# Optimization experiments

Hardware: AMD Instinct MI355X
Metric: run time of the kernel (lower is better)

Reference implementation:

```python
import jax, jax.numpy as jnp
import numpy as np

PAD, UNK, START = 0, 1, 2
V, E, H = 32000, 256, 512   # vocab, emb dim, encoder hidden per direction
H2 = 2 * H                   # decoder hidden / encoder output dim
B, L, T = 32, 400, 64
OOV = 100


def _lstm(xe, Wi, Wh, b, reverse=False):
    """xe: [B,L,E] -> (hs [B,L,H], h_last [B,H])."""
    Bb = xe.shape[0]
    Hh = Wh.shape[0]
    def step(carry, xt):
        h, c = carry
        z = xt @ Wi + h @ Wh + b
        i, fg, g, o = jnp.split(z, 4, axis=-1)
        c = jax.nn.sigmoid(fg) * c + jax.nn.sigmoid(i) * jnp.tanh(g)
        h = jax.nn.sigmoid(o) * jnp.tanh(c)
        return (h, c), h
    init = (jnp.zeros((Bb, Hh), xe.dtype), jnp.zeros((Bb, Hh), xe.dtype))
    (hN, _), hs = jax.lax.scan(step, init, jnp.swapaxes(xe, 0, 1), reverse=reverse)
    return jnp.swapaxes(hs, 0, 1), hN


def _gru(x, h, Wi, Wh, b):
    D = h.shape[-1]
    zi = x @ Wi + b
    zh = h @ Wh
    r = jax.nn.sigmoid(zi[:, :D] + zh[:, :D])
    z = jax.nn.sigmoid(zi[:, D:2 * D] + zh[:, D:2 * D])
    n = jnp.tanh(zi[:, 2 * D:] + r * zh[:, 2 * D:])
    return (1.0 - z) * n + z * h


def _forward(embedding, enc_Wi_f, enc_Wh_f, enc_b_f, enc_Wi_b, enc_Wh_b, enc_b_b,
             dec_Wi, dec_Wh, dec_b, W_enc_att, W_dec_att, Wv, bv, Wp, bp,
             x, target_y, extend_vocab):
    Bb, Ll = x.shape
    Tt = target_y.shape[1]
    Vv = embedding.shape[0]
    Hh2 = dec_Wh.shape[0]
    xe = embedding[x]                                           # B,L,E
    hs_f, hN_f = _lstm(xe, enc_Wi_f, enc_Wh_f, enc_b_f)
    hs_b, hN_b = _lstm(xe, enc_Wi_b, enc_Wh_b, enc_b_b, reverse=True)
    enc_out = jnp.concatenate([hs_f, hs_b], axis=-1)            # B,L,2H
    dec_h0 = jnp.concatenate([hN_f, hN_b], axis=-1)             # B,2H
    bidx = jnp.arange(Bb)[:, None]

    def step(carry, inp):
        dec_in, dec_h, acc, prebuf = carry
        i, tgt = inp
        emb = embedding[dec_in]                                 # B,E
        dec_h = _gru(emb, dec_h, dec_Wi, dec_Wh, dec_b)         # B,2H
        # temporal encoder attention (normalize exp scores by running sum)
        e = jnp.einsum('bh,hk,blk->bl', dec_h, W_enc_att, enc_out)
        ee = jnp.exp(e)
        att_un = jnp.where(i == 0, ee, ee / (acc + 1e-10))
        acc = acc + ee
        enc_att = att_un / jnp.sum(att_un, axis=-1, keepdims=True)   # B,L
        enc_ctx = jnp.einsum('bl,blh->bh', enc_att, enc_out)
        # intra-decoder attention over previous decoder hiddens
        ed = jnp.einsum('bh,hk,btk->bt', dec_h, W_dec_att, prebuf)
        dmask = (jnp.arange(prebuf.shape[1]) < i)[None, :]
        dec_att = jax.nn.softmax(jnp.where(dmask, ed, -1e9), axis=-1)
        dec_ctx = jnp.einsum('bt,bth->bh', dec_att, prebuf)
        dec_ctx = jnp.where(i > 0, dec_ctx, 0.0)
        cat = jnp.concatenate([dec_h, enc_ctx, dec_ctx], axis=-1)    # B,6H
        p_gen = jax.nn.sigmoid(cat @ Wp + bp)                        # B,1
        ptr_dist = p_gen * enc_att                                   # B,L
        vocab_dist = (1.0 - p_gen) * jax.nn.softmax(cat @ Wv + bv, axis=-1)
        final = jnp.zeros((Bb, Vv + OOV), vocab_dist.dtype)
        final = final.at[:, :Vv].set(vocab_dist)
        final = final.at[bidx, extend_vocab].add(ptr_dist)           # copy mechanism
        dec_out = jnp.argmax(final, axis=-1)
        step_loss = -jnp.log(final[jnp.arange(Bb), tgt] + 1e-12)
        step_loss = step_loss * (tgt != PAD).astype(final.dtype)
        prebuf = jax.lax.dynamic_update_slice(prebuf, dec_h[:, None, :], (0, i, 0))
        nxt = jnp.where(dec_out >= Vv, UNK, dec_out).astype(dec_in.dtype)
        return (nxt, dec_h, acc, prebuf), (dec_out, step_loss)

    init = (jnp.full((Bb,), START, dtype=x.dtype), dec_h0,
            jnp.zeros((Bb, Ll), enc_out.dtype),
            jnp.zeros((Bb, Tt, Hh2), enc_out.dtype))
    _, (ys, losses) = jax.lax.scan(step, init, (jnp.arange(Tt), target_y.T))
    return jnp.swapaxes(ys, 0, 1), jnp.swapaxes(losses, 0, 1)


def setup_inputs() -> dict:
    key = jax.random.key(0)
    ks = jax.random.split(key, 16)
    s = 0.02
    nrm = lambda k, shape: jax.random.normal(k, shape, jnp.float32) * s
    return {
        'x': jax.random.randint(ks[0], (B, L), 0, V),
        'seq_len': L,
        'target_y': jax.random.randint(ks[1], (B, T), 0, V),
        'extend_vocab': jax.random.randint(ks[2], (B, L), 0, V + OOV),
        'max_ovv_len': OOV,
        'embedding': nrm(ks[3], (V, E)),
        'enc_Wi_f': nrm(ks[4], (E, 4 * H)),
        'enc_Wh_f': nrm(ks[5], (H, 4 * H)),
        'enc_b_f': jnp.zeros((4 * H,), jnp.float32),
        'enc_Wi_b': nrm(ks[6], (E, 4 * H)),
        'enc_Wh_b': nrm(ks[7], (H, 4 * H)),
        'enc_b_b': jnp.zeros((4 * H,), jnp.float32),
        'dec_Wi': nrm(ks[8], (E, 3 * H2)),
        'dec_Wh': nrm(ks[9], (H2, 3 * H2)),
        'dec_b': jnp.zeros((3 * H2,), jnp.float32),
        'W_enc_att': nrm(ks[10], (H2, H2)),
        'W_dec_att': nrm(ks[11], (H2, H2)),
        'Wv': nrm(ks[12], (3 * H2, V)),
        'bv': jnp.zeros((V,), jnp.float32),
        'Wp': nrm(ks[13], (3 * H2, 1)),
        'bp': jnp.zeros((1,), jnp.float32),
    }


def reference(x, seq_len, target_y, extend_vocab, max_ovv_len,
              embedding, enc_Wi_f, enc_Wh_f, enc_b_f, enc_Wi_b, enc_Wh_b, enc_b_b,
              dec_Wi, dec_Wh, dec_b, W_enc_att, W_dec_att, Wv, bv, Wp, bp):
    return _forward(embedding, enc_Wi_f, enc_Wh_f, enc_b_f, enc_Wi_b, enc_Wh_b, enc_b_b,
                    dec_Wi, dec_Wh, dec_b, W_enc_att, W_dec_att, Wv, bv, Wp, bp,
                    x, target_y, extend_vocab)
```

## Files before the change

kernel.cpp:

```cpp
#include <hip/hip_runtime.h>
#include <math.h>

#define Bb 32
#define Lmax 400
#define Tt 64
#define Ee 256
#define Hh 512
#define H2 1024
#define Vv 32000
#define OOV 100
#define VX (Vv+OOV)
#define PAD_ID 0
#define UNK_ID 1
#define START_ID 2

__device__ __forceinline__ float sigf(float x){ return 1.0f/(1.0f+expf(-x)); }
__device__ __forceinline__ float bf2f(unsigned int u){ u <<= 16; return __uint_as_float(u); }

__global__ __launch_bounds__(256) void pack_enc_k(
    const float* __restrict__ Wi_f, const float* __restrict__ Wh_f, const float* __restrict__ b_f,
    const float* __restrict__ Wi_b, const float* __restrict__ Wh_b, const float* __restrict__ b_b,
    float4* __restrict__ wip, float4* __restrict__ whp, float4* __restrict__ bp)
{
  int o = blockIdx.x*256 + threadIdx.x;
  if (o < 2*256*512) {
    int n = o & 511; int k = (o >> 9) & 255; int dir = o >> 17;
    const float* W = dir ? Wi_b : Wi_f;
    wip[o] = make_float4(W[k*2048+n], W[k*2048+512+n], W[k*2048+1024+n], W[k*2048+1536+n]);
  }
  if (o < 2*512*512) {
    int n = o & 511; int k = (o >> 9) & 511; int dir = o >> 18;
    const float* W = dir ? Wh_b : Wh_f;
    whp[o] = make_float4(W[k*2048+n], W[k*2048+512+n], W[k*2048+1024+n], W[k*2048+1536+n]);
  }
  if (o < 2*512) {
    int n = o & 511; int dir = o >> 9;
    const float* bs = dir ? b_b : b_f;
    bp[o] = make_float4(bs[n], bs[512+n], bs[1024+n], bs[1536+n]);
  }
}

__global__ __launch_bounds__(512) void enc_step2_k(
    const float4* __restrict__ wip, const float4* __restrict__ whp, const float4* __restrict__ bp,
    const float* __restrict__ emb, const int* __restrict__ x,
    float* __restrict__ c_buf, float* __restrict__ enc_out, int t)
{
  __shared__ float4 wi_s[256*4];
  __shared__ float4 wh_s[512*4];
  __shared__ float4 red_s[4*128];
  int bx = blockIdx.x;
  int dir = bx >> 7, ng = bx & 127;
  int tid = threadIdx.x;
  int b = tid & 31, nl = (tid >> 5) & 3, ks = tid >> 7;
  int n = ng*4 + nl;
  for (int i = tid; i < 1024; i += 512) {
    int k = i >> 2, l = i & 3;
    wi_s[i] = wip[(dir*256 + k)*512 + ng*4 + l];
  }
  for (int i = tid; i < 2048; i += 512) {
    int k = i >> 2, l = i & 3;
    wh_s[i] = whp[(dir*512 + k)*512 + ng*4 + l];
  }
  __syncthreads();
  int tt = dir ? (Lmax-1-t) : t;
  int tok = x[b*Lmax + tt];
  const float* xr = emb + (size_t)tok*Ee;
  float4 acc = make_float4(0.f,0.f,0.f,0.f);
  if (t > 0) {
    int pt = dir ? (tt+1) : (tt-1);
    const float4* hb4 = (const float4*)(enc_out + ((size_t)b*Lmax + pt)*H2 + dir*Hh);
    #pragma unroll 4
    for (int k4 = ks*32; k4 < ks*32+32; ++k4) {
      float4 hv = hb4[k4];
      float4 w0 = wh_s[(k4*4+0)*4 + nl];
      float4 w1 = wh_s[(k4*4+1)*4 + nl];
      float4 w2 = wh_s[(k4*4+2)*4 + nl];
      float4 w3 = wh_s[(k4*4+3)*4 + nl];
      acc.x = fmaf(hv.x,w0.x,acc.x); acc.y = fmaf(hv.x,w0.y,acc.y);
      acc.z = fmaf(hv.x,w0.z,acc.z); acc.w = fmaf(hv.x,w0.w,acc.w);
      acc.x = fmaf(hv.y,w1.x,acc.x); acc.y = fmaf(hv.y,w1.y,acc.y);
      acc.z = fmaf(hv.y,w1.z,acc.z); acc.w = fmaf(hv.y,w1.w,acc.w);
      acc.x = fmaf(hv.z,w2.x,acc.x); acc.y = fmaf(hv.z,w2.y,acc.y);
      acc.z = fmaf(hv.z,w2.z,acc.z); acc.w = fmaf(hv.z,w2.w,acc.w);
      acc.x = fmaf(hv.w,w3.x,acc.x); acc.y = fmaf(hv.w,w3.y,acc.y);
      acc.z = fmaf(hv.w,w3.z,acc.z); acc.w = fmaf(hv.w,w3.w,acc.w);
    }
  }
  const float4* xr4 = (const float4*)xr;
  #pragma unroll 4
  for (int k4 = ks*16; k4 < ks*16+16; ++k4) {
    float4 xv = xr4[k4];
    float4 w0 = wi_s[(k4*4+0)*4 + nl];
    float4 w1 = wi_s[(k4*4+1)*4 + nl];
    float4 w2 = wi_s[(k4*4+2)*4 + nl];
    float4 w3 = wi_s[(k4*4+3)*4 + nl];
    acc.x = fmaf(xv.x,w0.x,acc.x); acc.y = fmaf(xv.x,w0.y,acc.y);
    acc.z = fmaf(xv.x,w0.z,acc.z); acc.w = fmaf(xv.x,w0.w,acc.w);
    acc.x = fmaf(xv.y,w1.x,acc.x); acc.y = fmaf(xv.y,w1.y,acc.y);
    acc.z = fmaf(xv.y,w1.z,acc.z); acc.w = fmaf(xv.y,w1.w,acc.w);
    acc.x = fmaf(xv.z,w2.x,acc.x); acc.y = fmaf(xv.z,w2.y,acc.y);
    acc.z = fmaf(xv.z,w2.z,acc.z); acc.w = fmaf(xv.z,w2.w,acc.w);
    acc.x = fmaf(xv.w,w3.x,acc.x); acc.y = fmaf(xv.w,w3.y,acc.y);
    acc.z = fmaf(xv.w,w3.z,acc.z); acc.w = fmaf(xv.w,w3.w,acc.w);
  }
  red_s[ks*128 + (tid & 127)] = acc;
  __syncthreads();
  if (tid < 128) {
    float4 a0 = red_s[tid], a1 = red_s[128+tid], a2 = red_s[256+tid], a3 = red_s[384+tid];
    float4 bb = bp[dir*512 + n];
    float zi = a0.x+a1.x+a2.x+a3.x + bb.x;
    float zf = a0.y+a1.y+a2.y+a3.y + bb.y;
    float zg = a0.z+a1.z+a2.z+a3.z + bb.z;
    float zo = a0.w+a1.w+a2.w+a3.w + bb.w;
    int ci = (dir*32 + b)*Hh + n;
    float cv = (t==0) ? 0.f : c_buf[ci];
    float cn = sigf(zf)*cv + sigf(zi)*tanhf(zg);
    float hn = sigf(zo)*tanhf(cn);
    c_buf[ci] = cn;
    enc_out[((size_t)b*Lmax + tt)*H2 + dir*Hh + n] = hn;
  }
}

__global__ __launch_bounds__(256) void init_dec_k(
    const float* __restrict__ enc_out, float* __restrict__ cat_buf, int* __restrict__ dec_in)
{
  int idx = blockIdx.x*256 + threadIdx.x;
  if (idx < Bb*H2) {
    int b = idx >> 10, n = idx & 1023;
    float v = (n < Hh) ? enc_out[((size_t)b*Lmax + (Lmax-1))*H2 + n]
                       : enc_out[(size_t)b*Lmax*H2 + n];
    cat_buf[b*3*H2 + n] = v;
  }
  if (idx < Bb) dec_in[idx] = START_ID;
}

__global__ __launch_bounds__(256) void gru_mm_k(
    const float* __restrict__ emb, const int* __restrict__ dec_in,
    const float* __restrict__ cat_buf, const float* __restrict__ Wi,
    const float* __restrict__ Wh, const float* __restrict__ bias,
    float* __restrict__ zi_buf, float* __restrict__ zh_buf)
{
  int bx = blockIdx.x;
  int ng = bx % 48; int bg = (bx / 48) & 7; int kq = bx / 384;
  int nl = threadIdx.x & 63, bl = threadIdx.x >> 6;
  int n = ng*64 + nl, b = bg*4 + bl;
  const float* hr = cat_buf + b*3*H2;
  float zh = 0.f;
  int k0 = kq*512;
  #pragma unroll 4
  for (int k = k0; k < k0+512; ++k)
    zh = fmaf(hr[k], Wh[(size_t)k*3*H2 + n], zh);
  zh_buf[(size_t)(kq*Bb + b)*3*H2 + n] = zh;
  if (kq == 0) {
    const float* er = emb + (size_t)dec_in[b]*Ee;
    float zi = bias[n];
    #pragma unroll 4
    for (int k = 0; k < Ee; ++k)
      zi = fmaf(er[k], Wi[(size_t)k*3*H2 + n], zi);
    zi_buf[b*3*H2 + n] = zi;
  }
}

__global__ __launch_bounds__(256) void gru_comb_k(
    const float* __restrict__ zi_buf, const float* __restrict__ zh_buf,
    float* __restrict__ cat_buf, float* __restrict__ prebuf, int t)
{
  int idx = blockIdx.x*256 + threadIdx.x;
  int b = idx >> 10, n = idx & 1023;
  const float* zi  = zi_buf + b*3*H2;
  const float* zh0 = zh_buf + (size_t)b*3*H2;
  const float* zh1 = zh_buf + (size_t)(Bb + b)*3*H2;
  float zhr = zh0[n]      + zh1[n];
  float zhz = zh0[H2+n]   + zh1[H2+n];
  float zhg = zh0[2*H2+n] + zh1[2*H2+n];
  float r  = sigf(zi[n] + zhr);
  float z  = sigf(zi[H2+n] + zhz);
  float nn = tanhf(zi[2*H2+n] + r*zhg);
  float hold = cat_buf[b*3*H2 + n];
  float h = (1.0f - z)*nn + z*hold;
  cat_buf[b*3*H2 + n] = h;
  prebuf[((size_t)b*Tt + t)*H2 + n] = h;
}

__global__ __launch_bounds__(256) void qq_k(
    const float* __restrict__ cat_buf, const float* __restrict__ Wea,
    const float* __restrict__ Wda, float* __restrict__ qp, float* __restrict__ qdp)
{
  int bx = blockIdx.x;
  int ng = bx & 15, bg = (bx >> 4) & 7, kq = bx >> 7;
  int nl = threadIdx.x & 63, bl = threadIdx.x >> 6;
  int n = ng*64 + nl, b = bg*4 + bl;
  const float* hr = cat_buf + b*3*H2 + kq*256;
  const float* wa = Wea + (size_t)(kq*256)*H2 + n;
  const float* wd = Wda + (size_t)(kq*256)*H2 + n;
  float s1 = 0.f, s2 = 0.f;
  #pragma unroll 4
  for (int k = 0; k < 256; ++k) {
    float hv = hr[k];
    s1 = fmaf(hv, wa[(size_t)k*H2], s1);
    s2 = fmaf(hv, wd[(size_t)k*H2], s2);
  }
  qp [(size_t)(kq*Bb + b)*H2 + n] = s1;
  qdp[(size_t)(kq*Bb + b)*H2 + n] = s2;
}

__global__ __launch_bounds__(256) void att_sc_k(
    const float* __restrict__ qp, const float* __restrict__ qdp,
    const float* __restrict__ enc_out, const float* __restrict__ prebuf,
    float* __restrict__ esc, float* __restrict__ ed, int t)
{
  int w = blockIdx.x*4 + (threadIdx.x >> 6);
  int lane = threadIdx.x & 63;
  int b = w / 464;
  int row = w - b*464;
  if (b >= Bb) return;
  float s = 0.0f;
  if (row < Lmax) {
    const float4* q0 = (const float4*)(qp + (size_t)(0*Bb + b)*H2);
    const float4* q1 = (const float4*)(qp + (size_t)(1*Bb + b)*H2);
    const float4* q2 = (const float4*)(qp + (size_t)(2*Bb + b)*H2);
    const float4* q3 = (const float4*)(qp + (size_t)(3*Bb + b)*H2);
    const float4* er = (const float4*)(enc_out + ((size_t)b*Lmax + row)*H2);
    #pragma unroll
    for (int j = 0; j < 4; ++j) {
      int idx = lane + 64*j;
      float4 a0 = q0[idx], a1 = q1[idx], a2 = q2[idx], a3 = q3[idx], e = er[idx];
      float ax = a0.x+a1.x+a2.x+a3.x;
      float ay = a0.y+a1.y+a2.y+a3.y;
      float az = a0.z+a1.z+a2.z+a3.z;
      float aw = a0.w+a1.w+a2.w+a3.w;
      s += ax*e.x + ay*e.y + az*e.z + aw*e.w;
    }
  } else {
    int tp = row - Lmax;
    if (tp >= t) { if (lane==0) ed[b*Tt+tp] = 0.0f; return; }
    const float4* q0 = (const float4*)(qdp + (size_t)(0*Bb + b)*H2);
    const float4* q1 = (const float4*)(qdp + (size_t)(1*Bb + b)*H2);
    const float4* q2 = (const float4*)(qdp + (size_t)(2*Bb + b)*H2);
    const float4* q3 = (const float4*)(qdp + (size_t)(3*Bb + b)*H2);
    const float4* pr = (const float4*)(prebuf + ((size_t)b*Tt + tp)*H2);
    #pragma unroll
    for (int j = 0; j < 4; ++j) {
      int idx = lane + 64*j;
      float4 a0 = q0[idx], a1 = q1[idx], a2 = q2[idx], a3 = q3[idx], e = pr[idx];
      float ax = a0.x+a1.x+a2.x+a3.x;
      float ay = a0.y+a1.y+a2.y+a3.y;
      float az = a0.z+a1.z+a2.z+a3.z;
      float aw = a0.w+a1.w+a2.w+a3.w;
      s += ax*e.x + ay*e.y + az*e.z + aw*e.w;
    }
  }
  for (int o = 32; o > 0; o >>= 1) s += __shfl_xor(s, o);
  if (lane == 0) { if (row < Lmax) esc[b*Lmax+row] = s; else ed[b*Tt + (row-Lmax)] = s; }
}

__global__ __launch_bounds__(256) void ctx_norm_k(
    const float* __restrict__ esc, const float* __restrict__ acc_r, float* __restrict__ acc_w,
    float* __restrict__ enc_att, const float* __restrict__ ed,
    const float* __restrict__ enc_out, const float* __restrict__ prebuf,
    float* __restrict__ cat_buf, int t)
{
  __shared__ float att_s[Lmax];
  __shared__ float datt_s[Tt];
  __shared__ float red[256];
  int b = blockIdx.x >> 4, kq = blockIdx.x & 15;
  int tid = threadIdx.x;
  float loc = 0.f;
  for (int l = tid; l < Lmax; l += 256) {
    float ee = expf(esc[b*Lmax + l]);
    float a  = (t == 0) ? 0.f : acc_r[b*Lmax + l];
    float un = (t == 0) ? ee : ee / (a + 1e-10f);
    att_s[l] = un;
    loc += un;
    if (kq == 0) acc_w[b*Lmax + l] = a + ee;
  }
  red[tid] = loc; __syncthreads();
  for (int s = 128; s > 0; s >>= 1) { if (tid < s) red[tid] += red[tid+s]; __syncthreads(); }
  float inv = 1.0f / red[0];
  for (int l = tid; l < Lmax; l += 256) {
    float v = att_s[l] * inv;
    att_s[l] = v;
    if (kq == 0) enc_att[b*Lmax + l] = v;
  }
  if (tid < 64 && t > 0) {
    float v = (tid < t) ? ed[b*Tt + tid] : -INFINITY;
    float m = v;
    for (int o = 32; o > 0; o >>= 1) m = fmaxf(m, __shfl_xor(m, o));
    float p = (tid < t) ? expf(v - m) : 0.f;
    float ss = p;
    for (int o = 32; o > 0; o >>= 1) ss += __shfl_xor(ss, o);
    datt_s[tid] = p / ss;
  }
  __syncthreads();
  int k = kq*64 + (tid & 63);
  int strip = tid >> 6;
  float ec = 0.f;
  const float* er = enc_out + (size_t)b*Lmax*H2 + k;
  #pragma unroll 4
  for (int l = strip; l < Lmax; l += 4)
    ec = fmaf(att_s[l], er[(size_t)l*H2], ec);
  float dc = 0.f;
  const float* pr = prebuf + (size_t)b*Tt*H2 + k;
  for (int tp = strip; tp < t; tp += 4)
    dc = fmaf(datt_s[tp], pr[(size_t)tp*H2], dc);
  __syncthreads();
  red[tid] = ec; __syncthreads();
  if (tid < 64)
    cat_buf[b*3*H2 + H2 + kq*64 + tid] = red[tid] + red[64+tid] + red[128+tid] + red[192+tid];
  __syncthreads();
  red[tid] = dc; __syncthreads();
  if (tid < 64)
    cat_buf[b*3*H2 + 2*H2 + kq*64 + tid] = red[tid] + red[64+tid] + red[128+tid] + red[192+tid];
}

__global__ __launch_bounds__(256) void pack_wv_k(const float* __restrict__ Wv, unsigned short* __restrict__ Wbf)
{
  size_t i = ((size_t)blockIdx.x*256 + threadIdx.x)*4;
  #pragma unroll
  for (int j = 0; j < 4; ++j) {
    unsigned int u = __float_as_uint(Wv[i+j]);
    u = (u + 0x7fffu + ((u >> 16) & 1u)) >> 16;
    Wbf[i+j] = (unsigned short)u;
  }
}

__global__ __launch_bounds__(256) void wv_mm_bf_k(
    const float* __restrict__ cat_buf, const unsigned short* __restrict__ Wbf,
    const float* __restrict__ bv, float* __restrict__ logits)
{
  __shared__ float As[32][33];
  __shared__ float Wsh[32][65];
  int tid = threadIdx.x;
  int n0 = blockIdx.x*64;
  int tx = tid & 15, ty = tid >> 4;
  float acc[2][4] = {};
  for (int k0 = 0; k0 < 3*H2; k0 += 32) {
    #pragma unroll
    for (int i = 0; i < 4; ++i) {
      int a = tid*4+i;
      As[a>>5][a&31] = cat_buf[(size_t)(a>>5)*3*H2 + k0 + (a&31)];
    }
    #pragma unroll
    for (int j = 0; j < 4; ++j) {
      int a = j*256 + tid;
      int row = a >> 5, c2 = (a & 31)*2;
      const unsigned int* wr = (const unsigned int*)(Wbf + (size_t)(k0+row)*Vv + n0);
      unsigned int u = wr[a & 31];
      Wsh[row][c2]   = bf2f(u & 0xffffu);
      Wsh[row][c2+1] = bf2f(u >> 16);
    }
    __syncthreads();
    #pragma unroll
    for (int kk = 0; kk < 32; ++kk) {
      float a0 = As[ty*2+0][kk], a1 = As[ty*2+1][kk];
      float w0 = Wsh[kk][tx*4+0], w1 = Wsh[kk][tx*4+1], w2 = Wsh[kk][tx*4+2], w3 = Wsh[kk][tx*4+3];
      acc[0][0]=fmaf(a0,w0,acc[0][0]); acc[0][1]=fmaf(a0,w1,acc[0][1]); acc[0][2]=fmaf(a0,w2,acc[0][2]); acc[0][3]=fmaf(a0,w3,acc[0][3]);
      acc[1][0]=fmaf(a1,w0,acc[1][0]); acc[1][1]=fmaf(a1,w1,acc[1][1]); acc[1][2]=fmaf(a1,w2,acc[1][2]); acc[1][3]=fmaf(a1,w3,acc[1][3]);
    }
    __syncthreads();
  }
  #pragma unroll
  for (int i = 0; i < 2; ++i)
    #pragma unroll
    for (int j = 0; j < 4; ++j) {
      int n = n0 + tx*4 + j;
      logits[(size_t)(ty*2+i)*Vv + n] = acc[i][j] + bv[n];
    }
}

__global__ __launch_bounds__(256) void wv_mm_k(
    const float* __restrict__ cat_buf, const float* __restrict__ Wv,
    const float* __restrict__ bv, float* __restrict__ logits)
{
  __shared__ float As[32][33];
  __shared__ float Wsh[32][128];
  int tid = threadIdx.x;
  int n0 = blockIdx.x*128;
  int tx = tid & 31, ty = tid >> 5;
  float acc[4][4] = {};
  for (int k0 = 0; k0 < 3*H2; k0 += 32) {
    #pragma unroll
    for (int i = 0; i < 4; ++i) {
      int a = tid*4+i;
      As[a>>5][a&31] = cat_buf[(size_t)(a>>5)*3*H2 + k0 + (a&31)];
    }
    #pragma unroll
    for (int j = 0; j < 16; ++j) {
      int a = j*256+tid;
      Wsh[a>>7][a&127] = Wv[(size_t)(k0+(a>>7))*Vv + n0 + (a&127)];
    }
    __syncthreads();
    #pragma unroll
    for (int kk = 0; kk < 32; ++kk) {
      float a0 = As[ty*4+0][kk], a1 = As[ty*4+1][kk], a2 = As[ty*4+2][kk], a3 = As[ty*4+3][kk];
      float w0 = Wsh[kk][tx*4+0], w1 = Wsh[kk][tx*4+1], w2 = Wsh[kk][tx*4+2], w3 = Wsh[kk][tx*4+3];
      acc[0][0]=fmaf(a0,w0,acc[0][0]); acc[0][1]=fmaf(a0,w1,acc[0][1]); acc[0][2]=fmaf(a0,w2,acc[0][2]); acc[0][3]=fmaf(a0,w3,acc[0][3]);
      acc[1][0]=fmaf(a1,w0,acc[1][0]); acc[1][1]=fmaf(a1,w1,acc[1][1]); acc[1][2]=fmaf(a1,w2,acc[1][2]); acc[1][3]=fmaf(a1,w3,acc[1][3]);
      acc[2][0]=fmaf(a2,w0,acc[2][0]); acc[2][1]=fmaf(a2,w1,acc[2][1]); acc[2][2]=fmaf(a2,w2,acc[2][2]); acc[2][3]=fmaf(a2,w3,acc[2][3]);
      acc[3][0]=fmaf(a3,w0,acc[3][0]); acc[3][1]=fmaf(a3,w1,acc[3][1]); acc[3][2]=fmaf(a3,w2,acc[3][2]); acc[3][3]=fmaf(a3,w3,acc[3][3]);
    }
    __syncthreads();
  }
  #pragma unroll
  for (int i = 0; i < 4; ++i)
    #pragma unroll
    for (int j = 0; j < 4; ++j) {
      int n = n0 + tx*4 + j;
      logits[(size_t)(ty*4+i)*Vv + n] = acc[i][j] + bv[n];
    }
}

__global__ __launch_bounds__(256) void final_k(
    const float* __restrict__ logits, const float* __restrict__ cat_buf,
    const float* __restrict__ Wp, const float* __restrict__ bps,
    const int* __restrict__ ev, const float* __restrict__ enc_att,
    const int* __restrict__ tgt_y, float* __restrict__ out,
    int* __restrict__ dec_in, int t)
{
  __shared__ float rf[256];
  __shared__ int   ri[256];
  __shared__ float tm[256];
  __shared__ int   ev_s[Lmax];
  __shared__ float pv_s[Lmax];
  __shared__ float m_sh, sc_sh, pg_sh;
  int b = blockIdx.x, tid = threadIdx.x;
  const float*  lr  = logits + (size_t)b*Vv;
  const float4* lr4 = (const float4*)lr;
  {
    const float* catr = cat_buf + b*3*H2;
    float pgl = 0.f;
    for (int i = tid; i < 3*H2; i += 256) pgl += catr[i]*Wp[i];
    rf[tid] = pgl; __syncthreads();
    for (int s = 128; s > 0; s >>= 1) { if (tid < s) rf[tid] += rf[tid+s]; __syncthreads(); }
    if (tid == 0) pg_sh = sigf(rf[0] + bps[0]);
    __syncthreads();
  }
  float m = -1e30f;
  for (int i = tid; i < Vv/4; i += 256) {
    float4 v = lr4[i];
    m = fmaxf(m, fmaxf(fmaxf(v.x,v.y), fmaxf(v.z,v.w)));
  }
  rf[tid] = m; __syncthreads();
  for (int s = 128; s > 0; s >>= 1) { if (tid < s) rf[tid] = fmaxf(rf[tid], rf[tid+s]); __syncthreads(); }
  m = rf[0]; __syncthreads();
  float ssum = 0.f;
  for (int i = tid; i < Vv/4; i += 256) {
    float4 v = lr4[i];
    ssum += expf(v.x-m) + expf(v.y-m) + expf(v.z-m) + expf(v.w-m);
  }
  rf[tid] = ssum; __syncthreads();
  for (int s = 128; s > 0; s >>= 1) { if (tid < s) rf[tid] += rf[tid+s]; __syncthreads(); }
  if (tid == 0) {
    sc_sh = (1.0f - pg_sh) / rf[0]; m_sh = m;
  }
  for (int l = tid; l < Lmax; l += 256) ev_s[l] = ev[b*Lmax + l];
  __syncthreads();
  float scale = sc_sh, pg = pg_sh; m = m_sh;
  for (int l = tid; l < Lmax; l += 256) pv_s[l] = pg * enc_att[b*Lmax + l];
  __syncthreads();
  float best = -1e30f; int bi = 0x7fffffff;
  for (int i = tid; i < Vv/4; i += 256) {
    float4 v = lr4[i];
    float p0 = expf(v.x-m)*scale, p1 = expf(v.y-m)*scale, p2 = expf(v.z-m)*scale, p3 = expf(v.w-m)*scale;
    int n = 4*i;
    if (p0 > best) { best = p0; bi = n; }
    if (p1 > best || (p1 == best && n+1 < bi)) { best = p1; bi = n+1; }
    if (p2 > best || (p2 == best && n+2 < bi)) { best = p2; bi = n+2; }
    if (p3 > best || (p3 == best && n+3 < bi)) { best = p3; bi = n+3; }
  }
  int tgt = tgt_y[b*Tt + t];
  float ptm = 0.f;
  for (int l = tid; l < Lmax; l += 256) {
    int e = ev_s[l];
    float tot = 0.f;
    for (int l2 = 0; l2 < Lmax; ++l2) if (ev_s[l2] == e) tot += pv_s[l2];
    float vvv = tot + ((e < Vv) ? expf(lr[e]-m)*scale : 0.f);
    if (vvv > best || (vvv == best && e < bi)) { best = vvv; bi = e; }
    ptm += (e == tgt) ? pv_s[l] : 0.f;
  }
  rf[tid] = best; ri[tid] = bi; tm[tid] = ptm; __syncthreads();
  for (int s = 128; s > 0; s >>= 1) {
    if (tid < s) {
      float v2 = rf[tid+s]; int i2 = ri[tid+s];
      if (v2 > rf[tid] || (v2 == rf[tid] && i2 < ri[tid])) { rf[tid] = v2; ri[tid] = i2; }
      tm[tid] += tm[tid+s];
    }
    __syncthreads();
  }
  if (tid == 0) {
    int am = ri[0];
    float fr_tgt = expf(lr[tgt]-m)*scale + tm[0];
    float loss = (tgt != PAD_ID) ? -logf(fr_tgt + 1e-12f) : 0.0f;
    out[b*Tt + t] = (float)am;
    out[Bb*Tt + b*Tt + t] = loss;
    dec_in[b] = (am >= Vv) ? UNK_ID : am;
  }
}

extern "C" void kernel_launch(void* const* d_in, const int* in_sizes, int n_in,
                              void* d_out, int out_size, void* d_ws, size_t ws_size,
                              hipStream_t stream)
{
  const int*   x    = (const int*)  d_in[0];
  const int*   tgt  = (const int*)  d_in[2];
  const int*   ev   = (const int*)  d_in[3];
  const float* emb  = (const float*)d_in[5];
  const float* Wi_f = (const float*)d_in[6];
  const float* Wh_f = (const float*)d_in[7];
  const float* b_f  = (const float*)d_in[8];
  const float* Wi_b = (const float*)d_in[9];
  const float* Wh_b = (const float*)d_in[10];
  const float* b_b  = (const float*)d_in[11];
  const float* dWi  = (const float*)d_in[12];
  const float* dWh  = (const float*)d_in[13];
  const float* db   = (const float*)d_in[14];
  const float* Wea  = (const float*)d_in[15];
  const float* Wda  = (const float*)d_in[16];
  const float* Wv   = (const float*)d_in[17];
  const float* bv   = (const float*)d_in[18];
  const float* Wp   = (const float*)d_in[19];
  const float* bp   = (const float*)d_in[20];
  float* out = (float*)d_out;

  float* ws = (float*)d_ws;
  size_t off = 0;
  float* enc_out = ws + off; off += (size_t)Bb*Lmax*H2;
  float* c_buf   = ws + off; off += 2*Bb*Hh;
  float4* wip    = (float4*)(ws + off); off += 2*256*512*4;
  float4* whp    = (float4*)(ws + off); off += 2*512*512*4;
  float4* biasp  = (float4*)(ws + off); off += 2*512*4;
  float* cat_buf = ws + off; off += Bb*3*H2;
  float* prebuf  = ws + off; off += (size_t)Bb*Tt*H2;
  float* accumA  = ws + off; off += Bb*Lmax;
  float* accumB  = ws + off; off += Bb*Lmax;
  float* zi_buf  = ws + off; off += Bb*3*H2;
  float* zh_buf  = ws + off; off += (size_t)2*Bb*3*H2;
  float* qp      = ws + off; off += (size_t)4*Bb*H2;
  float* qdp     = ws + off; off += (size_t)4*Bb*H2;
  float* esc     = ws + off; off += Bb*Lmax;
  float* enc_att = ws + off; off += Bb*Lmax;
  float* ed      = ws + off; off += Bb*Tt;
  float* logits  = ws + off; off += (size_t)Bb*Vv;
  int*   dec_in  = (int*)(ws + off); off += 32;
  unsigned short* Wbf = (unsigned short*)(ws + off);
  size_t need_bf16 = off*4 + (size_t)3*H2*Vv*2;
  int use_bf16 = (ws_size >= need_bf16 + (64u<<10)) ? 1 : 0;

  pack_enc_k<<<2048,256,0,stream>>>(Wi_f,Wh_f,b_f,Wi_b,Wh_b,b_b,wip,whp,biasp);
  if (use_bf16) pack_wv_k<<<96000,256,0,stream>>>(Wv, Wbf);

  for (int t = 0; t < Lmax; ++t)
    enc_step2_k<<<256,512,0,stream>>>(wip,whp,biasp,emb,x,c_buf,enc_out,t);

  init_dec_k<<<128,256,0,stream>>>(enc_out,cat_buf,dec_in);

  for (int t = 0; t < Tt; ++t) {
    float* ar = (t & 1) ? accumB : accumA;
    float* aw = (t & 1) ? accumA : accumB;
    gru_mm_k  <<<768,256,0,stream>>>(emb,dec_in,cat_buf,dWi,dWh,db,zi_buf,zh_buf);
    gru_comb_k<<<128,256,0,stream>>>(zi_buf,zh_buf,cat_buf,prebuf,t);
    qq_k      <<<512,256,0,stream>>>(cat_buf,Wea,Wda,qp,qdp);
    att_sc_k  <<<3712,256,0,stream>>>(qp,qdp,enc_out,prebuf,esc,ed,t);
    ctx_norm_k<<<512,256,0,stream>>>(esc,ar,aw,enc_att,ed,enc_out,prebuf,cat_buf,t);
    if (use_bf16) wv_mm_bf_k<<<500,256,0,stream>>>(cat_buf,Wbf,bv,logits);
    else          wv_mm_k   <<<250,256,0,stream>>>(cat_buf,Wv,bv,logits);
    final_k   <<<32,256,0,stream>>>(logits,cat_buf,Wp,bp,ev,enc_att,tgt,out,dec_in,t);
  }
}
```

Before: 37.15 ms.

## Register-tile encoder LSTM step over batch and fuse GRU combine into attention projection

The encoder step kernel now stages the previous hidden states and embeddings for all 32 batch rows in shared memory. Each thread computes 4 batch rows and reuses each loaded weight float4 across them, with a 16-way k-split reduction through shared memory. The GRU combine kernel is folded into the query-projection kernel, which recomputes the new hidden state per block, and a small qsum kernel pre-reduces the four k-split partial projections. This removes redundant partial sums in the 3712-block attention-score kernel. The costs are more shared memory per encoder block, which may limit occupancy, and redundant GRU gate computation across the 16 column groups.

```diff
diff --git a/kernel.cpp b/kernel.cpp
--- a/kernel.cpp
+++ b/kernel.cpp
@@ -40,19 +40,34 @@
   }
 }
 
-__global__ __launch_bounds__(512) void enc_step2_k(
+#define FMA16(ACC, HV, W0, W1, W2, W3) \
+  ACC.x = fmaf(HV.x, W0.x, ACC.x); ACC.y = fmaf(HV.x, W0.y, ACC.y); \
+  ACC.z = fmaf(HV.x, W0.z, ACC.z); ACC.w = fmaf(HV.x, W0.w, ACC.w); \
+  ACC.x = fmaf(HV.y, W1.x, ACC.x); ACC.y = fmaf(HV.y, W1.y, ACC.y); \
+  ACC.z = fmaf(HV.y, W1.z, ACC.z); ACC.w = fmaf(HV.y, W1.w, ACC.w); \
+  ACC.x = fmaf(HV.z, W2.x, ACC.x); ACC.y = fmaf(HV.z, W2.y, ACC.y); \
+  ACC.z = fmaf(HV.z, W2.z, ACC.z); ACC.w = fmaf(HV.z, W2.w, ACC.w); \
+  ACC.x = fmaf(HV.w, W3.x, ACC.x); ACC.y = fmaf(HV.w, W3.y, ACC.y); \
+  ACC.z = fmaf(HV.w, W3.z, ACC.z); ACC.w = fmaf(HV.w, W3.w, ACC.w);
+
+__global__ __launch_bounds__(512) void enc_step3_k(
     const float4* __restrict__ wip, const float4* __restrict__ whp, const float4* __restrict__ bp,
     const float* __restrict__ emb, const int* __restrict__ x,
     float* __restrict__ c_buf, float* __restrict__ enc_out, int t)
 {
   __shared__ float4 wi_s[256*4];
   __shared__ float4 wh_s[512*4];
-  __shared__ float4 red_s[4*128];
+  __shared__ float4 hs2[128*33];
+  __shared__ float4 xr_red[64*33];
   int bx = blockIdx.x;
   int dir = bx >> 7, ng = bx & 127;
   int tid = threadIdx.x;
-  int b = tid & 31, nl = (tid >> 5) & 3, ks = tid >> 7;
-  int n = ng*4 + nl;
+  int ks = tid >> 5;
+  int r  = tid & 31;
+  int bq = r & 7, nl = r >> 3;
+  int b0 = bq*4;
+  int tt = dir ? (Lmax-1-t) : t;
+
   for (int i = tid; i < 1024; i += 512) {
     int k = i >> 2, l = i & 3;
     wi_s[i] = wip[(dir*256 + k)*512 + ng*4 + l];
@@ -61,57 +76,91 @@
     int k = i >> 2, l = i & 3;
     wh_s[i] = whp[(dir*512 + k)*512 + ng*4 + l];
   }
-  __syncthreads();
-  int tt = dir ? (Lmax-1-t) : t;
-  int tok = x[b*Lmax + tt];
-  const float* xr = emb + (size_t)tok*Ee;
-  float4 acc = make_float4(0.f,0.f,0.f,0.f);
+  {
+    int sb = tid >> 4, kb = tid & 15;
+    int tok = x[sb*Lmax + tt];
+    const float4* er = (const float4*)(emb + (size_t)tok*Ee);
+    #pragma unroll
+    for (int i = 0; i < 4; ++i) {
+      int k4 = kb + 16*i;
+      xr_red[k4*33 + sb] = er[k4];
+    }
+  }
   if (t > 0) {
     int pt = dir ? (tt+1) : (tt-1);
-    const float4* hb4 = (const float4*)(enc_out + ((size_t)b*Lmax + pt)*H2 + dir*Hh);
-    #pragma unroll 4
-    for (int k4 = ks*32; k4 < ks*32+32; ++k4) {
-      float4 hv = hb4[k4];
+    int sb = tid >> 4, kb = tid & 15;
+    const float4* hb = (const float4*)(enc_out + ((size_t)sb*Lmax + pt)*H2 + dir*Hh);
+    #pragma unroll
+    for (int i = 0; i < 8; ++i) {
+      int k4 = kb + 16*i;
+      hs2[k4*33 + sb] = hb[k4];
+    }
+  }
+  __syncthreads();
+
+  float4 acc0 = make_float4(0.f,0.f,0.f,0.f);
+  float4 acc1 = acc0, acc2 = acc0, acc3 = acc0;
+  if (t > 0) {
+    int k4b = ks*8;
+    #pragma unroll
+    for (int kk = 0; kk < 8; ++kk) {
+      int k4 = k4b + kk;
       float4 w0 = wh_s[(k4*4+0)*4 + nl];
       float4 w1 = wh_s[(k4*4+1)*4 + nl];
       float4 w2 = wh_s[(k4*4+2)*4 + nl];
       float4 w3 = wh_s[(k4*4+3)*4 + nl];
-      acc.x = fmaf(hv.x,w0.x,acc.x); acc.y = fmaf(hv.x,w0.y,acc.y);
-      acc.z = fmaf(hv.x,w0.z,acc.z); acc.w = fmaf(hv.x,w0.w,acc.w);
-      acc.x = fmaf(hv.y,w1.x,acc.x); acc.y = fmaf(hv.y,w1.y,acc.y);
-      acc.z = fmaf(hv.y,w1.z,acc.z); acc.w = fmaf(hv.y,w1.w,acc.w);
-      acc.x = fmaf(hv.z,w2.x,acc.x); acc.y = fmaf(hv.z,w2.y,acc.y);
-      acc.z = fmaf(hv.z,w2.z,acc.z); acc.w = fmaf(hv.z,w2.w,acc.w);
-      acc.x = fmaf(hv.w,w3.x,acc.x); acc.y = fmaf(hv.w,w3.y,acc.y);
-      acc.z = fmaf(hv.w,w3.z,acc.z); acc.w = fmaf(hv.w,w3.w,acc.w);
-    }
-  }
-  const float4* xr4 = (const float4*)xr;
-  #pragma unroll 4
-  for (int k4 = ks*16; k4 < ks*16+16; ++k4) {
-    float4 xv = xr4[k4];
-    float4 w0 = wi_s[(k4*4+0)*4 + nl];
-    float4 w1 = wi_s[(k4*4+1)*4 + nl];
-    float4 w2 = wi_s[(k4*4+2)*4 + nl];
-    float4 w3 = wi_s[(k4*4+3)*4 + nl];
-    acc.x = fmaf(xv.x,w0.x,acc.x); acc.y = fmaf(xv.x,w0.y,acc.y);
-    acc.z = fmaf(xv.x,w0.z,acc.z); acc.w = fmaf(xv.x,w0.w,acc.w);
-    acc.x = fmaf(xv.y,w1.x,acc.x); acc.y = fmaf(xv.y,w1.y,acc.y);
-    acc.z = fmaf(xv.y,w1.z,acc.z); acc.w = fmaf(xv.y,w1.w,acc.w);
-    acc.x = fmaf(xv.z,w2.x,acc.x); acc.y = fmaf(xv.z,w2.y,acc.y);
-    acc.z = fmaf(xv.z,w2.z,acc.z); acc.w = fmaf(xv.z,w2.w,acc.w);
-    acc.x = fmaf(xv.w,w3.x,acc.x); acc.y = fmaf(xv.w,w3.y,acc.y);
-    acc.z = fmaf(xv.w,w3.z,acc.z); acc.w = fmaf(xv.w,w3.w,acc.w);
-  }
-  red_s[ks*128 + (tid & 127)] = acc;
+      float4 h0 = hs2[k4*33 + b0+0];
+      float4 h1 = hs2[k4*33 + b0+1];
+      float4 h2 = hs2[k4*33 + b0+2];
+      float4 h3 = hs2[k4*33 + b0+3];
+      FMA16(acc0, h0, w0, w1, w2, w3);
+      FMA16(acc1, h1, w0, w1, w2, w3);
+      FMA16(acc2, h2, w0, w1, w2, w3);
+      FMA16(acc3, h3, w0, w1, w2, w3);
+    }
+  }
+  {
+    int k4b = ks*4;
+    #pragma unroll
+    for (int kk = 0; kk < 4; ++kk) {
+      int k4 = k4b + kk;
+      float4 w0 = wi_s[(k4*4+0)*4 + nl];
+      float4 w1 = wi_s[(k4*4+1)*4 + nl];
+      float4 w2 = wi_s[(k4*4+2)*4 + nl];
+      float4 w3 = wi_s[(k4*4+3)*4 + nl];
+      float4 h0 = xr_red[k4*33 + b0+0];
+      float4 h1 = xr_red[k4*33 + b0+1];
+      float4 h2 = xr_red[k4*33 + b0+2];
+      float4 h3 = xr_red[k4*33 + b0+3];
+      FMA16(acc0, h0, w0, w1, w2, w3);
+      FMA16(acc1, h1, w0, w1, w2, w3);
+      FMA16(acc2, h2, w0, w1, w2, w3);
+      FMA16(acc3, h3, w0, w1, w2, w3);
+    }
+  }
+  __syncthreads();
+  {
+    int base = ks*132 + 16*bq + nl;
+    xr_red[base + 0]  = acc0;
+    xr_red[base + 4]  = acc1;
+    xr_red[base + 8]  = acc2;
+    xr_red[base + 12] = acc3;
+  }
   __syncthreads();
   if (tid < 128) {
-    float4 a0 = red_s[tid], a1 = red_s[128+tid], a2 = red_s[256+tid], a3 = red_s[384+tid];
+    int bn = tid;
+    float4 s = xr_red[bn];
+    #pragma unroll
+    for (int kr = 1; kr < 16; ++kr) {
+      float4 v = xr_red[kr*132 + bn];
+      s.x += v.x; s.y += v.y; s.z += v.z; s.w += v.w;
+    }
+    int b = bn >> 2, nl2 = bn & 3, n = ng*4 + nl2;
     float4 bb = bp[dir*512 + n];
-    float zi = a0.x+a1.x+a2.x+a3.x + bb.x;
-    float zf = a0.y+a1.y+a2.y+a3.y + bb.y;
-    float zg = a0.z+a1.z+a2.z+a3.z + bb.z;
-    float zo = a0.w+a1.w+a2.w+a3.w + bb.w;
+    float zi = s.x + bb.x;
+    float zf = s.y + bb.y;
+    float zg = s.z + bb.z;
+    float zo = s.w + bb.w;
     int ci = (dir*32 + b)*Hh + n;
     float cv = (t==0) ? 0.f : c_buf[ci];
     float cn = sigf(zf)*cv + sigf(zi)*tanhf(zg);
@@ -122,7 +171,8 @@
 }
 
 __global__ __launch_bounds__(256) void init_dec_k(
-    const float* __restrict__ enc_out, float* __restrict__ cat_buf, int* __restrict__ dec_in)
+    const float* __restrict__ enc_out, float* __restrict__ cat_buf,
+    float* __restrict__ h0, int* __restrict__ dec_in)
 {
   int idx = blockIdx.x*256 + threadIdx.x;
   if (idx < Bb*H2) {
@@ -130,6 +180,7 @@
     float v = (n < Hh) ? enc_out[((size_t)b*Lmax + (Lmax-1))*H2 + n]
                        : enc_out[(size_t)b*Lmax*H2 + n];
     cat_buf[b*3*H2 + n] = v;
+    h0[b*H2 + n] = v;
   }
   if (idx < Bb) dec_in[idx] = START_ID;
 }
@@ -161,51 +212,70 @@
   }
 }
 
-__global__ __launch_bounds__(256) void gru_comb_k(
+__global__ __launch_bounds__(256) void qq_f_k(
     const float* __restrict__ zi_buf, const float* __restrict__ zh_buf,
-    float* __restrict__ cat_buf, float* __restrict__ prebuf, int t)
-{
-  int idx = blockIdx.x*256 + threadIdx.x;
-  int b = idx >> 10, n = idx & 1023;
-  const float* zi  = zi_buf + b*3*H2;
-  const float* zh0 = zh_buf + (size_t)b*3*H2;
-  const float* zh1 = zh_buf + (size_t)(Bb + b)*3*H2;
-  float zhr = zh0[n]      + zh1[n];
-  float zhz = zh0[H2+n]   + zh1[H2+n];
-  float zhg = zh0[2*H2+n] + zh1[2*H2+n];
-  float r  = sigf(zi[n] + zhr);
-  float z  = sigf(zi[H2+n] + zhz);
-  float nn = tanhf(zi[2*H2+n] + r*zhg);
-  float hold = cat_buf[b*3*H2 + n];
-  float h = (1.0f - z)*nn + z*hold;
-  cat_buf[b*3*H2 + n] = h;
-  prebuf[((size_t)b*Tt + t)*H2 + n] = h;
-}
-
-__global__ __launch_bounds__(256) void qq_k(
-    const float* __restrict__ cat_buf, const float* __restrict__ Wea,
-    const float* __restrict__ Wda, float* __restrict__ qp, float* __restrict__ qdp)
-{
+    const float* __restrict__ h0, float* __restrict__ prebuf,
+    const float* __restrict__ Wea, const float* __restrict__ Wda,
+    float* __restrict__ cat_buf, float* __restrict__ qp, float* __restrict__ qdp, int t)
+{
+  __shared__ float hsq[4*260];
   int bx = blockIdx.x;
   int ng = bx & 15, bg = (bx >> 4) & 7, kq = bx >> 7;
   int nl = threadIdx.x & 63, bl = threadIdx.x >> 6;
   int n = ng*64 + nl, b = bg*4 + bl;
-  const float* hr = cat_buf + b*3*H2 + kq*256;
+  const float* zi  = zi_buf + b*3*H2;
+  const float* zh0 = zh_buf + (size_t)b*3*H2;
+  const float* zh1 = zh_buf + (size_t)(Bb + b)*3*H2;
+  #pragma unroll
+  for (int i = 0; i < 4; ++i) {
+    int kk = nl + 64*i, k = kq*256 + kk;
+    float zhr = zh0[k]      + zh1[k];
+    float zhz = zh0[H2+k]   + zh1[H2+k];
+    float zhg = zh0[2*H2+k] + zh1[2*H2+k];
+    float rr = sigf(zi[k] + zhr);
+    float zz = sigf(zi[H2+k] + zhz);
+    float nn = tanhf(zi[2*H2+k] + rr*zhg);
+    float hold = (t == 0) ? h0[b*H2 + k]
+                          : prebuf[((size_t)b*Tt + (t-1))*H2 + k];
+    float h = (1.0f - zz)*nn + zz*hold;
+    hsq[bl*260 + kk] = h;
+    if (ng == 0) {
+      cat_buf[b*3*H2 + k] = h;
+      prebuf[((size_t)b*Tt + t)*H2 + k] = h;
+    }
+  }
+  __syncthreads();
+  const float* hr = hsq + bl*260;
   const float* wa = Wea + (size_t)(kq*256)*H2 + n;
   const float* wd = Wda + (size_t)(kq*256)*H2 + n;
   float s1 = 0.f, s2 = 0.f;
   #pragma unroll 4
-  for (int k = 0; k < 256; ++k) {
-    float hv = hr[k];
-    s1 = fmaf(hv, wa[(size_t)k*H2], s1);
-    s2 = fmaf(hv, wd[(size_t)k*H2], s2);
+  for (int kk = 0; kk < 256; ++kk) {
+    float hv = hr[kk];
+    s1 = fmaf(hv, wa[(size_t)kk*H2], s1);
+    s2 = fmaf(hv, wd[(size_t)kk*H2], s2);
   }
   qp [(size_t)(kq*Bb + b)*H2 + n] = s1;
   qdp[(size_t)(kq*Bb + b)*H2 + n] = s2;
 }
 
+__global__ __launch_bounds__(256) void qsum_k(
+    const float* __restrict__ qp, const float* __restrict__ qdp,
+    float* __restrict__ q, float* __restrict__ qd)
+{
+  int i = blockIdx.x*256 + threadIdx.x;
+  const float4* p  = (const float4*)qp;
+  const float4* pd = (const float4*)qdp;
+  float4 a = p[i], b1 = p[8192+i], c = p[16384+i], d = p[24576+i];
+  ((float4*)q)[i] = make_float4(a.x+b1.x+c.x+d.x, a.y+b1.y+c.y+d.y,
+                                a.z+b1.z+c.z+d.z, a.w+b1.w+c.w+d.w);
+  float4 e = pd[i], f = pd[8192+i], g = pd[16384+i], h = pd[24576+i];
+  ((float4*)qd)[i] = make_float4(e.x+f.x+g.x+h.x, e.y+f.y+g.y+h.y,
+                                 e.z+f.z+g.z+h.z, e.w+f.w+g.w+h.w);
+}
+
 __global__ __launch_bounds__(256) void att_sc_k(
-    const float* __restrict__ qp, const float* __restrict__ qdp,
+    const float* __restrict__ q, const float* __restrict__ qd,
     const float* __restrict__ enc_out, const float* __restrict__ prebuf,
     float* __restrict__ esc, float* __restrict__ ed, int t)
 {
@@ -216,38 +286,22 @@
   if (b >= Bb) return;
   float s = 0.0f;
   if (row < Lmax) {
-    const float4* q0 = (const float4*)(qp + (size_t)(0*Bb + b)*H2);
-    const float4* q1 = (const float4*)(qp + (size_t)(1*Bb + b)*H2);
-    const float4* q2 = (const float4*)(qp + (size_t)(2*Bb + b)*H2);
-    const float4* q3 = (const float4*)(qp + (size_t)(3*Bb + b)*H2);
+    const float4* qr = (const float4*)(q + b*H2);
     const float4* er = (const float4*)(enc_out + ((size_t)b*Lmax + row)*H2);
     #pragma unroll
     for (int j = 0; j < 4; ++j) {
-      int idx = lane + 64*j;
-      float4 a0 = q0[idx], a1 = q1[idx], a2 = q2[idx], a3 = q3[idx], e = er[idx];
-      float ax = a0.x+a1.x+a2.x+a3.x;
-      float ay = a0.y+a1.y+a2.y+a3.y;
-      float az = a0.z+a1.z+a2.z+a3.z;
-      float aw = a0.w+a1.w+a2.w+a3.w;
-      s += ax*e.x + ay*e.y + az*e.z + aw*e.w;
+      float4 a = qr[lane + 64*j], e = er[lane + 64*j];
+      s += a.x*e.x + a.y*e.y + a.z*e.z + a.w*e.w;
     }
   } else {
     int tp = row - Lmax;
     if (tp >= t) { if (lane==0) ed[b*Tt+tp] = 0.0f; return; }
-    const float4* q0 = (const float4*)(qdp + (size_t)(0*Bb + b)*H2);
-    const float4* q1 = (const float4*)(qdp + (size_t)(1*Bb + b)*H2);
-    const float4* q2 = (const float4*)(qdp + (size_t)(2*Bb + b)*H2);
-    const float4* q3 = (const float4*)(qdp + (size_t)(3*Bb + b)*H2);
+    const float4* qr = (const float4*)(qd + b*H2);
     const float4* pr = (const float4*)(prebuf + ((size_t)b*Tt + tp)*H2);
     #pragma unroll
     for (int j = 0; j < 4; ++j) {
-      int idx = lane + 64*j;
-      float4 a0 = q0[idx], a1 = q1[idx], a2 = q2[idx], a3 = q3[idx], e = pr[idx];
-      float ax = a0.x+a1.x+a2.x+a3.x;
-      float ay = a0.y+a1.y+a2.y+a3.y;
-      float az = a0.z+a1.z+a2.z+a3.z;
-      float aw = a0.w+a1.w+a2.w+a3.w;
-      s += ax*e.x + ay*e.y + az*e.z + aw*e.w;
+      float4 a = qr[lane + 64*j], e = pr[lane + 64*j];
+      s += a.x*e.x + a.y*e.y + a.z*e.z + a.w*e.w;
     }
   }
   for (int o = 32; o > 0; o >>= 1) s += __shfl_xor(s, o);
@@ -537,6 +591,9 @@
   float* zh_buf  = ws + off; off += (size_t)2*Bb*3*H2;
   float* qp      = ws + off; off += (size_t)4*Bb*H2;
   float* qdp     = ws + off; off += (size_t)4*Bb*H2;
+  float* q       = ws + off; off += Bb*H2;
+  float* qd      = ws + off; off += Bb*H2;
+  float* h0      = ws + off; off += Bb*H2;
   float* esc     = ws + off; off += Bb*Lmax;
   float* enc_att = ws + off; off += Bb*Lmax;
   float* ed      = ws + off; off += Bb*Tt;
@@ -550,17 +607,17 @@
   if (use_bf16) pack_wv_k<<<96000,256,0,stream>>>(Wv, Wbf);
 
   for (int t = 0; t < Lmax; ++t)
-    enc_step2_k<<<256,512,0,stream>>>(wip,whp,biasp,emb,x,c_buf,enc_out,t);
-
-  init_dec_k<<<128,256,0,stream>>>(enc_out,cat_buf,dec_in);
+    enc_step3_k<<<256,512,0,stream>>>(wip,whp,biasp,emb,x,c_buf,enc_out,t);
+
+  init_dec_k<<<128,256,0,stream>>>(enc_out,cat_buf,h0,dec_in);
 
   for (int t = 0; t < Tt; ++t) {
     float* ar = (t & 1) ? accumB : accumA;
     float* aw = (t & 1) ? accumA : accumB;
     gru_mm_k  <<<768,256,0,stream>>>(emb,dec_in,cat_buf,dWi,dWh,db,zi_buf,zh_buf);
-    gru_comb_k<<<128,256,0,stream>>>(zi_buf,zh_buf,cat_buf,prebuf,t);
-    qq_k      <<<512,256,0,stream>>>(cat_buf,Wea,Wda,qp,qdp);
-    att_sc_k  <<<3712,256,0,stream>>>(qp,qdp,enc_out,prebuf,esc,ed,t);
+    qq_f_k    <<<512,256,0,stream>>>(zi_buf,zh_buf,h0,prebuf,Wea,Wda,cat_buf,qp,qdp,t);
+    qsum_k    <<<32,256,0,stream>>>(qp,qdp,q,qd);
+    att_sc_k  <<<3712,256,0,stream>>>(q,qd,enc_out,prebuf,esc,ed,t);
     ctx_norm_k<<<512,256,0,stream>>>(esc,ar,aw,enc_att,ed,enc_out,prebuf,cat_buf,t);
     if (use_bf16) wv_mm_bf_k<<<500,256,0,stream>>>(cat_buf,Wbf,bv,logits);
     else          wv_mm_k   <<<250,256,0,stream>>>(cat_buf,Wv,bv,logits);
```

Result: faster. 34.72 ms (-6.5%).
